# Kernel tuning notes

Measured on AMD Instinct MI355X. Metric: run time of the kernel, lower is better.

## Reference

```python
import jax, jax.numpy as jnp
import numpy as np

B = 262144
STEPS = 15            # Program.steps = var(15)
SPEED = 5.0           # Program.straight_speed
TRAJ_IDX = np.array([10, 1, 2, 3, 4, 5, 6, 7, 8, 17])
FEAT_IDX = np.array([1, 2, 3, 4, 9, 17])


def setup_inputs() -> dict:
    key = jax.random.key(0)
    ks = jax.random.split(key, 9)
    x = jax.random.normal(ks[0], (B, 18), dtype=jnp.float32)
    x = x.at[:, 0].set(0.0)  # loop counter i starts at 0 -> exactly 15 iterations
    return {
        "x": x,
        "c1w": jax.random.normal(ks[1], (2,), jnp.float32) * 0.5,
        "c1b": jax.random.normal(ks[2], (1,), jnp.float32) * 0.1,
        "c2w": jax.random.normal(ks[3], (2,), jnp.float32) * 0.5,
        "c2b": jax.random.normal(ks[4], (1,), jnp.float32) * 0.1,
        "l1w": jax.random.normal(ks[5], (4, 32), jnp.float32) * 0.3,
        "l1b": jax.random.normal(ks[6], (32,), jnp.float32) * 0.1,
        "l2w": jax.random.normal(ks[7], (32, 5), jnp.float32) * 0.3,
        "l2b": jax.random.normal(ks[8], (5,), jnp.float32) * 0.1,
    }


def _classifier(feat, c1w, c1b, c2w, c2b, l1w, l1b, l2w, l2b):
    # feat: [B,6] -> conv1d(k=2): [B,5] -> conv1d(k=2): [B,4] -> 32 -> 5, sigmoid
    h = jax.nn.relu(c1w[0] * feat[:, :-1] + c1w[1] * feat[:, 1:] + c1b)
    h = jax.nn.relu(c2w[0] * h[:, :-1] + c2w[1] * h[:, 1:] + c2b)
    h = jax.nn.relu(h @ l1w + l1b)
    return jax.nn.sigmoid(h @ l2w + l2b)  # [B,5]


def _distance(s):
    return (s[:, 1] - s[:, 3]) ** 2 + (s[:, 2] - s[:, 4]) ** 2


def _program(x, c1w, c1b, c2w, c2b, l1w, l1b, l2w, l2b):
    s = x.at[:, 10].set(_distance(x))          # initial assign_distance
    traj0 = s[:, TRAJ_IDX]                      # initial trajectory_update

    def step(s, _):
        # assign_branch_probability
        p = _classifier(s[:, FEAT_IDX], c1w, c1b, c2w, c2b, l1w, l1b, l2w, l2b)
        s = (s.at[:, 5].set(p[:, 0]).at[:, 6].set(p[:, 1]).at[:, 7].set(p[:, 2])
              .at[:, 8].set(p[:, 3]).at[:, 17].set(p[:, 4]))
        p5, p6, p7, p8 = p[:, 0], p[:, 1], p[:, 2], p[:, 3]
        # assign_comparison_block: pairwise diffs a..f at indices 11..16
        a, b, c = p6 - p5, p7 - p5, p8 - p5
        d, e, f = p7 - p6, p8 - p6, p8 - p7
        s = (s.at[:, 11].set(a).at[:, 12].set(b).at[:, 13].set(c)
              .at[:, 14].set(d).at[:, 15].set(e).at[:, 16].set(f))
        # ifelse_argmax_ITE: nested compare against comparison_bar=0.0
        dx_c = jnp.where(c <= 0.0, 0.0, SPEED);  st_c = jnp.where(c <= 0.0, 0.0, 3.0)   # cruise vs right
        dx_f = jnp.where(f <= 0.0, 0.0, SPEED);  st_f = jnp.where(f <= 0.0, 2.0, 3.0)   # straight vs right
        dx_e = jnp.where(e <= 0.0, -SPEED, SPEED); st_e = jnp.where(e <= 0.0, 1.0, 3.0)  # left vs right
        dx_b = jnp.where(b <= 0.0, dx_c, dx_f);  st_b = jnp.where(b <= 0.0, st_c, st_f)
        dx_d = jnp.where(d <= 0.0, dx_e, dx_f);  st_d = jnp.where(d <= 0.0, st_e, st_f)
        dx   = jnp.where(a <= 0.0, dx_b, dx_d);  st   = jnp.where(a <= 0.0, st_b, st_d)
        s = s.at[:, 1].add(dx).at[:, 9].set(st)
        # assign_y1, assign_x2, assign_update_i, assign_distance
        s = s.at[:, 2].add(SPEED).at[:, 3].add(SPEED).at[:, 0].add(1.0)
        s = s.at[:, 10].set(_distance(s))
        return s, s[:, TRAJ_IDX]

    s, recs = jax.lax.scan(step, s, None, length=STEPS)
    traj = jnp.concatenate([traj0[:, None, :], jnp.moveaxis(recs, 0, 1)], axis=1)  # [B,16,10]
    return jnp.concatenate([s, traj.reshape(s.shape[0], -1)], axis=1)  # [B, 18+160]


def reference(x, c1w, c1b, c2w, c2b, l1w, l1b, l2w, l2b):
    return _program(x, c1w, c1b, c2w, c2b, l1w, l1b, l2w, l2b)
```

## Files before the change

### kernel.cpp

```cpp
#include <hip/hip_runtime.h>


constexpr int kB     = 262144;
constexpr int kSteps = 15;

__device__ __forceinline__ float relu_(float v) { return fmaxf(v, 0.0f); }
__device__ __forceinline__ float sigmoid_(float v) {
    return __builtin_amdgcn_rcpf(1.0f + __expf(-v));
}

__global__ __launch_bounds__(256) void Program_4578435138231_kernel(
    const float* __restrict__ x,
    const float* __restrict__ c1w, const float* __restrict__ c1b,
    const float* __restrict__ c2w, const float* __restrict__ c2b,
    const float* __restrict__ l1w, const float* __restrict__ l1b,
    const float* __restrict__ l2w, const float* __restrict__ l2b,
    float* __restrict__ out)
{
    const int i = blockIdx.x * 256 + threadIdx.x;
    if (i >= kB) return;

    const float2* xr = reinterpret_cast<const float2*>(x + (size_t)i * 18);
    float s[18];
    #pragma unroll
    for (int j = 0; j < 9; ++j) {
        float2 v = xr[j];
        s[2 * j]     = v.x;
        s[2 * j + 1] = v.y;
    }

    const float cw10 = c1w[0], cw11 = c1w[1], cb1 = c1b[0];
    const float cw20 = c2w[0], cw21 = c2w[1], cb2 = c2b[0];

    {
        float dA = s[1] - s[3], dB = s[2] - s[4];
        s[10] = dA * dA + dB * dB;
    }

    float* orow = out + (size_t)i * 178;

    {
        float2* tr = reinterpret_cast<float2*>(orow + 18);
        tr[0] = make_float2(s[10], s[1]);
        tr[1] = make_float2(s[2],  s[3]);
        tr[2] = make_float2(s[4],  s[5]);
        tr[3] = make_float2(s[6],  s[7]);
        tr[4] = make_float2(s[8],  s[17]);
    }

    #pragma unroll 1
    for (int t = 0; t < kSteps; ++t) {
        float f0 = s[1], f1 = s[2], f2 = s[3], f3 = s[4], f4 = s[9], f5 = s[17];
        float h10 = relu_(cw10 * f0 + cw11 * f1 + cb1);
        float h11 = relu_(cw10 * f1 + cw11 * f2 + cb1);
        float h12 = relu_(cw10 * f2 + cw11 * f3 + cb1);
        float h13 = relu_(cw10 * f3 + cw11 * f4 + cb1);
        float h14 = relu_(cw10 * f4 + cw11 * f5 + cb1);
        float g0 = relu_(cw20 * h10 + cw21 * h11 + cb2);
        float g1 = relu_(cw20 * h11 + cw21 * h12 + cb2);
        float g2 = relu_(cw20 * h12 + cw21 * h13 + cb2);
        float g3 = relu_(cw20 * h13 + cw21 * h14 + cb2);

        float p0 = l2b[0], p1 = l2b[1], p2 = l2b[2], p3 = l2b[3], p4 = l2b[4];
        #pragma unroll
        for (int k = 0; k < 32; ++k) {
            float h = g0 * l1w[k] + g1 * l1w[32 + k] + g2 * l1w[64 + k]
                    + g3 * l1w[96 + k] + l1b[k];
            h = relu_(h);
            p0 += h * l2w[5 * k + 0];
            p1 += h * l2w[5 * k + 1];
            p2 += h * l2w[5 * k + 2];
            p3 += h * l2w[5 * k + 3];
            p4 += h * l2w[5 * k + 4];
        }
        p0 = sigmoid_(p0); p1 = sigmoid_(p1); p2 = sigmoid_(p2);
        p3 = sigmoid_(p3); p4 = sigmoid_(p4);

        s[5] = p0; s[6] = p1; s[7] = p2; s[8] = p3; s[17] = p4;
        float a = p1 - p0, b = p2 - p0, c = p3 - p0;
        float d = p2 - p1, e = p3 - p1, f = p3 - p2;
        s[11] = a; s[12] = b; s[13] = c; s[14] = d; s[15] = e; s[16] = f;

        float dx_c = (c <= 0.f) ? 0.f  : 5.f,  st_c = (c <= 0.f) ? 0.f : 3.f;
        float dx_f = (f <= 0.f) ? 0.f  : 5.f,  st_f = (f <= 0.f) ? 2.f : 3.f;
        float dx_e = (e <= 0.f) ? -5.f : 5.f,  st_e = (e <= 0.f) ? 1.f : 3.f;
        float dx_b = (b <= 0.f) ? dx_c : dx_f, st_b = (b <= 0.f) ? st_c : st_f;
        float dx_d = (d <= 0.f) ? dx_e : dx_f, st_d = (d <= 0.f) ? st_e : st_f;
        float dx   = (a <= 0.f) ? dx_b : dx_d, st   = (a <= 0.f) ? st_b : st_d;

        s[1] += dx; s[9] = st;
        s[2] += 5.f; s[3] += 5.f; s[0] += 1.f;
        float dA = s[1] - s[3], dB = s[2] - s[4];
        s[10] = dA * dA + dB * dB;

        float2* tr = reinterpret_cast<float2*>(orow + 18 + 10 * (t + 1));
        tr[0] = make_float2(s[10], s[1]);
        tr[1] = make_float2(s[2],  s[3]);
        tr[2] = make_float2(s[4],  s[5]);
        tr[3] = make_float2(s[6],  s[7]);
        tr[4] = make_float2(s[8],  s[17]);
    }

    float2* os = reinterpret_cast<float2*>(orow);
    #pragma unroll
    for (int j = 0; j < 9; ++j) os[j] = make_float2(s[2 * j], s[2 * j + 1]);
}

extern "C" void kernel_launch(void* const* d_in, const int* in_sizes, int n_in,
                              void* d_out, int out_size, void* d_ws, size_t ws_size,
                              hipStream_t stream) {
    const float* x   = (const float*)d_in[0];
    const float* c1w = (const float*)d_in[1];
    const float* c1b = (const float*)d_in[2];
    const float* c2w = (const float*)d_in[3];
    const float* c2b = (const float*)d_in[4];
    const float* l1w = (const float*)d_in[5];
    const float* l1b = (const float*)d_in[6];
    const float* l2w = (const float*)d_in[7];
    const float* l2b = (const float*)d_in[8];
    float* out = (float*)d_out;

    Program_4578435138231_kernel<<<kB / 256, 256, 0, stream>>>(
        x, c1w, c1b, c2w, c2b, l1w, l1b, l2w, l2b, out);
}
```

Before: 299.0 us.

## Stage input loads and trajectory stores through LDS for coalesced global access

```diff
diff --git a/kernel.cpp b/kernel.cpp
--- a/kernel.cpp
+++ b/kernel.cpp
@@ -3,6 +3,7 @@
 
 constexpr int kB     = 262144;
 constexpr int kSteps = 15;
+constexpr int PAD    = 33;
 
 __device__ __forceinline__ float relu_(float v) { return fmaxf(v, 0.0f); }
 __device__ __forceinline__ float sigmoid_(float v) {
@@ -17,17 +18,26 @@
     const float* __restrict__ l2w, const float* __restrict__ l2b,
     float* __restrict__ out)
 {
-    const int i = blockIdx.x * 256 + threadIdx.x;
-    if (i >= kB) return;
+    __shared__ float lds[256 * PAD];
+    const int tid = threadIdx.x;
+    const int R0  = blockIdx.x * 256;
 
-    const float2* xr = reinterpret_cast<const float2*>(x + (size_t)i * 18);
+    {
+        const float* xblk = x + (size_t)R0 * 18;
+        #pragma unroll
+        for (int j = 0; j < 18; ++j) {
+            int flat = tid + 256 * j;
+            float v  = xblk[flat];
+            int r = (int)(((unsigned)flat * 58255u) >> 20);
+            int c = flat - r * 18;
+            lds[r * PAD + c] = v;
+        }
+    }
+    __syncthreads();
     float s[18];
     #pragma unroll
-    for (int j = 0; j < 9; ++j) {
-        float2 v = xr[j];
-        s[2 * j]     = v.x;
-        s[2 * j + 1] = v.y;
-    }
+    for (int j = 0; j < 18; ++j) s[j] = lds[tid * PAD + j];
+    __syncthreads();
 
     const float cw10 = c1w[0], cw11 = c1w[1], cb1 = c1b[0];
     const float cw20 = c2w[0], cw21 = c2w[1], cb2 = c2b[0];
@@ -37,16 +47,25 @@
         s[10] = dA * dA + dB * dB;
     }
 
-    float* orow = out + (size_t)i * 178;
+    float* lr = lds + tid * PAD;
 
-    {
-        float2* tr = reinterpret_cast<float2*>(orow + 18);
-        tr[0] = make_float2(s[10], s[1]);
-        tr[1] = make_float2(s[2],  s[3]);
-        tr[2] = make_float2(s[4],  s[5]);
-        tr[3] = make_float2(s[6],  s[7]);
-        tr[4] = make_float2(s[8],  s[17]);
-    }
+    auto flush32 = [&](int wcol) {
+        __syncthreads();
+        const int rr = tid >> 5, cc = tid & 31;
+        const float* lp = lds + rr * PAD + cc;
+        float*       op = out + (size_t)(R0 + rr) * 178 + wcol + cc;
+        #pragma unroll
+        for (int j = 0; j < 32; ++j) {
+            op[(size_t)(8 * j) * 178] = lp[8 * j * PAD];
+        }
+        __syncthreads();
+    };
+
+    int wstart = 18;
+    int nextb  = 50;
+
+    lr[0] = s[10]; lr[1] = s[1];  lr[2] = s[2]; lr[3] = s[3]; lr[4] = s[4];
+    lr[5] = s[5];  lr[6] = s[6];  lr[7] = s[7]; lr[8] = s[8]; lr[9] = s[17];
 
     #pragma unroll 1
     for (int t = 0; t < kSteps; ++t) {
@@ -93,17 +112,58 @@
         float dA = s[1] - s[3], dB = s[2] - s[4];
         s[10] = dA * dA + dB * dB;
 
-        float2* tr = reinterpret_cast<float2*>(orow + 18 + 10 * (t + 1));
-        tr[0] = make_float2(s[10], s[1]);
-        tr[1] = make_float2(s[2],  s[3]);
-        tr[2] = make_float2(s[4],  s[5]);
-        tr[3] = make_float2(s[6],  s[7]);
-        tr[4] = make_float2(s[8],  s[17]);
+        float v0 = s[10], v1 = s[1], v2 = s[2], v3 = s[3], v4 = s[4];
+        float v5 = s[5],  v6 = s[6], v7 = s[7], v8 = s[8], v9 = s[17];
+        const int c0 = 28 + 10 * t;
+        const int kk = nextb - c0;
+        int off = c0 - wstart;
+        if (kk >= 10) {
+            lr[off + 0] = v0; lr[off + 1] = v1; lr[off + 2] = v2;
+            lr[off + 3] = v3; lr[off + 4] = v4; lr[off + 5] = v5;
+            lr[off + 6] = v6; lr[off + 7] = v7; lr[off + 8] = v8;
+            lr[off + 9] = v9;
+            if (kk == 10) {
+                flush32(wstart);
+                wstart = nextb; nextb += 32;
+            }
+        } else {
+            if (kk > 0) lr[off + 0] = v0;
+            if (kk > 1) lr[off + 1] = v1;
+            if (kk > 2) lr[off + 2] = v2;
+            if (kk > 3) lr[off + 3] = v3;
+            if (kk > 4) lr[off + 4] = v4;
+            if (kk > 5) lr[off + 5] = v5;
+            if (kk > 6) lr[off + 6] = v6;
+            if (kk > 7) lr[off + 7] = v7;
+            if (kk > 8) lr[off + 8] = v8;
+            if (kk > 9) lr[off + 9] = v9;
+            flush32(wstart);
+            wstart = nextb; nextb += 32;
+            off = c0 - wstart;
+            if (kk <= 0) lr[off + 0] = v0;
+            if (kk <= 1) lr[off + 1] = v1;
+            if (kk <= 2) lr[off + 2] = v2;
+            if (kk <= 3) lr[off + 3] = v3;
+            if (kk <= 4) lr[off + 4] = v4;
+            if (kk <= 5) lr[off + 5] = v5;
+            if (kk <= 6) lr[off + 6] = v6;
+            if (kk <= 7) lr[off + 7] = v7;
+            if (kk <= 8) lr[off + 8] = v8;
+            if (kk <= 9) lr[off + 9] = v9;
+        }
     }
 
-    float2* os = reinterpret_cast<float2*>(orow);
+    __syncthreads();
     #pragma unroll
-    for (int j = 0; j < 9; ++j) os[j] = make_float2(s[2 * j], s[2 * j + 1]);
+    for (int j = 0; j < 18; ++j) lr[j] = s[j];
+    __syncthreads();
+    #pragma unroll
+    for (int j = 0; j < 18; ++j) {
+        int flat = tid + 256 * j;
+        int r = (int)(((unsigned)flat * 58255u) >> 20);
+        int c = flat - r * 18;
+        out[(size_t)(R0 + r) * 178 + c] = lds[r * PAD + c];
+    }
 }
 
 extern "C" void kernel_launch(void* const* d_in, const int* in_sizes, int n_in,
```

Result: faster. 285.3 us (-4.6%).
